# Kernel tuning notes

Measured on AMD Instinct MI355X. Metric: run time of the kernel, lower is better.

The kernel has to match this reference:

```python
import jax, jax.numpy as jnp
import numpy as np

N = 1_000_000   # samples
D_IN = 100      # covariate dim (cfg_density[0][0])
H = 64          # hidden dim
NUM_HEADS = 5   # t-bins [0,.2,.4,.6,.8,1.0]


def setup_inputs() -> dict:
    key = jax.random.key(0)
    ks = jax.random.split(key, 17)
    s = 0.05  # param scale for numerical stability (torch init is data-independent anyway)
    return {
        "t": jax.random.uniform(ks[0], (N,), dtype=jnp.float32),
        "x": jax.random.normal(ks[1], (N, D_IN), dtype=jnp.float32),
        # density feature MLP (two Linear+ReLU layers)
        "dW1": jax.random.normal(ks[2], (D_IN, H), dtype=jnp.float32) * s,
        "db1": jax.random.normal(ks[3], (H,), dtype=jnp.float32) * s,
        "dW2": jax.random.normal(ks[4], (H, H), dtype=jnp.float32) * s,
        "db2": jax.random.normal(ks[5], (H,), dtype=jnp.float32) * s,
        # 5 multi-head branches, each 3 Treat_Linear layers (istreat=1 since isenhance=1)
        "hw1": jax.random.normal(ks[6], (NUM_HEADS, H, H), dtype=jnp.float32) * s,
        "htw1": jax.random.normal(ks[7], (NUM_HEADS, H), dtype=jnp.float32) * s,
        "hb1": jax.random.normal(ks[8], (NUM_HEADS, H), dtype=jnp.float32) * s,
        "hw2": jax.random.normal(ks[9], (NUM_HEADS, H, H), dtype=jnp.float32) * s,
        "htw2": jax.random.normal(ks[10], (NUM_HEADS, H), dtype=jnp.float32) * s,
        "hb2": jax.random.normal(ks[11], (NUM_HEADS, H), dtype=jnp.float32) * s,
        "hw3": jax.random.normal(ks[12], (NUM_HEADS, H, 1), dtype=jnp.float32) * s,
        "htw3": jax.random.normal(ks[13], (NUM_HEADS, 1), dtype=jnp.float32) * s,
        "hb3": jax.random.normal(ks[14], (NUM_HEADS, 1), dtype=jnp.float32) * s,
    }


def reference(t, x, dW1, db1, dW2, db2,
              hw1, htw1, hb1, hw2, htw2, hb2, hw3, htw3, hb3):
    # hidden_features: Linear+ReLU, Linear+ReLU
    h = jax.nn.relu(x @ dW1 + db1)        # [N, H]
    h = jax.nn.relu(h @ dW2 + db2)        # [N, H]

    tt = t[:, None]                        # treatment column [N, 1]
    # bin index per row: t in [0.2*q, 0.2*(q+1)); last bin closed at 1.0
    bins = jnp.clip(jnp.floor(t * NUM_HEADS).astype(jnp.int32), 0, NUM_HEADS - 1)

    out = jnp.zeros((x.shape[0], 1), dtype=h.dtype)
    for q in range(NUM_HEADS):  # fixed small set of structurally-distinct heads
        # Treat_Linear layer 1: feat@W + t*tw + b, relu
        a = jax.nn.relu(h @ hw1[q] + tt * htw1[q] + hb1[q])
        # Treat_Linear layer 2
        a = jax.nn.relu(a @ hw2[q] + tt * htw2[q] + hb2[q])
        # last layer: no activation, islastlayer=1
        a = a @ hw3[q] + tt * htw3[q] + hb3[q]   # [N, 1]
        out = out + jnp.where((bins == q)[:, None], a, 0.0)
    return out  # Drnet returns (None, Q); g is None so we return Q
```

## Files before the change

kernel.cpp:

```cpp
#include <hip/hip_runtime.h>

typedef _Float16 f16;
typedef _Float16 f16x8 __attribute__((ext_vector_type(8)));
typedef float f32x4 __attribute__((ext_vector_type(4)));

#define NB 5
#define H 64
#define DIN 100
#define NT 256
#define MAIN_BLOCKS 512

#define FR_W1   0
#define FR_W2   1024
#define FR_HD   1536
#define FR_TOT  6656

__global__ __launch_bounds__(256)
void prepack_kernel(const float* __restrict__ dW1, const float* __restrict__ dW2,
                    const float* __restrict__ hw1, const float* __restrict__ hw2,
                    f16x8* __restrict__ pw)
{
    int F = blockIdx.x * 256 + threadIdx.x;
    if (F >= FR_TOT) return;
    int lane = F & 63, g = lane >> 4, c = lane & 15;
    const float* src;
    int s, mt, kmax;
    if (F < FR_W2) {
        int r = F; s = r >> 8; mt = (r >> 6) & 3; src = dW1; kmax = 100;
    } else if (F < FR_HD) {
        int r = F - FR_W2; s = r >> 8; mt = (r >> 6) & 3; src = dW2; kmax = 64;
    } else {
        int r = F - FR_HD; int ql = r >> 9; int q = ql >> 1; int l = ql & 1;
        int r2 = r & 511; s = r2 >> 8; mt = (r2 >> 6) & 3;
        src = (l ? hw2 : hw1) + q * 64 * 64; kmax = 64;
    }
    f16x8 v;
    #pragma unroll
    for (int e = 0; e < 8; ++e) {
        int k = 32 * s + 8 * g + e;
        int m = 16 * mt + c;
        float val = (k < kmax) ? src[k * 64 + m] : 0.0f;
        v[e] = (f16)val;
    }
    pw[F] = v;
}

__device__ __forceinline__ f32x4 mfma16(f16x8 a, f16x8 b, f32x4 c) {
    return __builtin_amdgcn_mfma_f32_16x16x32_f16(a, b, c, 0, 0, 0);
}

__global__ __launch_bounds__(NT, 2)
void drnet_main(const float* __restrict__ t, const float* __restrict__ x,
                const float* __restrict__ db1, const float* __restrict__ db2,
                const float* __restrict__ hb1, const float* __restrict__ htw1,
                const float* __restrict__ hb2, const float* __restrict__ htw2,
                const float* __restrict__ hw3, const float* __restrict__ htw3,
                const float* __restrict__ hb3,
                const f16x8* __restrict__ pw,
                float* __restrict__ out, int N, int nch)
{
    __shared__ float sb1f[H], sb2f[H];
    __shared__ float shb1[NB * H], shw1t[NB * H], shb2[NB * H], shw2t[NB * H], sw3f[NB * H];
    __shared__ float shtw3[NB], shb3[NB];
    __shared__ unsigned char sli[NT], sqv[NT];
    __shared__ float stv[NT];
    __shared__ int scnt[NB + 1], sbase[NB + 1];
    __shared__ __align__(16) unsigned char hbuf[4][2][2048];

    const int tid = threadIdx.x;
    const int lane = tid & 63;
    const int wv = tid >> 6;
    const int g = lane >> 4;
    const int row = lane & 15;

    for (int p = tid; p < H; p += NT) { sb1f[p] = db1[p]; sb2f[p] = db2[p]; }
    for (int p = tid; p < NB * H; p += NT) {
        shb1[p] = hb1[p];  shw1t[p] = htw1[p];
        shb2[p] = hb2[p];  shw2t[p] = htw2[p];
        sw3f[p] = hw3[p];
    }
    if (tid < NB) { shtw3[tid] = htw3[tid]; shb3[tid] = hb3[tid]; }

    f16x8 w1f[16], w2f[8];
    #pragma unroll
    for (int u = 0; u < 16; ++u) w1f[u] = pw[FR_W1 + u * 64 + lane];
    #pragma unroll
    for (int u = 0; u < 8; ++u)  w2f[u] = pw[FR_W2 + u * 64 + lane];

    for (int ch = blockIdx.x; ch < nch; ch += MAIN_BLOCKS) {
        __syncthreads();
        if (tid <= NB) scnt[tid] = 0;
        __syncthreads();
        const int i0 = ch * NT + tid;
        int q0 = NB; float tv0 = 0.f;
        if (i0 < N) {
            tv0 = t[i0];
            int b = (int)floorf(tv0 * 5.0f);
            q0 = min(max(b, 0), NB - 1);
        }
        int pos = atomicAdd(&scnt[q0], 1);
        __syncthreads();
        if (tid == 0) {
            int r = 0;
            #pragma unroll
            for (int b = 0; b <= NB; ++b) { sbase[b] = r; r += scnt[b]; }
        }
        __syncthreads();
        int sp = sbase[q0] + pos;
        sli[sp] = (unsigned char)tid; sqv[sp] = (unsigned char)q0; stv[sp] = tv0;
        __syncthreads();

        for (int j = 0; j < 4; ++j) {
            const int p0 = (wv * 4 + j) * 16;
            const int qlo = sqv[p0];
            if (qlo >= NB) continue;
            const int qhi = min((int)sqv[p0 + 15], NB - 1);
            const int li = sli[p0 + row];
            const int rq = sqv[p0 + row];
            const float rt = stv[p0 + row];
            const int iv = (rq < NB) ? (ch * NT + li) : (ch * NT);

            const float4* x4 = (const float4*)(x + (size_t)iv * DIN);
            f16x8 xf[4];
            #pragma unroll
            for (int s = 0; s < 3; ++s) {
                float4 a = x4[8 * s + 2 * g];
                float4 b = x4[8 * s + 2 * g + 1];
                xf[s][0] = (f16)a.x; xf[s][1] = (f16)a.y; xf[s][2] = (f16)a.z; xf[s][3] = (f16)a.w;
                xf[s][4] = (f16)b.x; xf[s][5] = (f16)b.y; xf[s][6] = (f16)b.z; xf[s][7] = (f16)b.w;
            }
            {
                float4 a = make_float4(0.f, 0.f, 0.f, 0.f);
                if (g == 0) a = x4[24];
                xf[3][0] = (f16)a.x; xf[3][1] = (f16)a.y; xf[3][2] = (f16)a.z; xf[3][3] = (f16)a.w;
                xf[3][4] = (f16)0.f; xf[3][5] = (f16)0.f; xf[3][6] = (f16)0.f; xf[3][7] = (f16)0.f;
            }
            const f32x4 zero = {0.f, 0.f, 0.f, 0.f};
            f32x4 acc[4] = {zero, zero, zero, zero};
            #pragma unroll
            for (int s = 0; s < 4; ++s)
                #pragma unroll
                for (int mt = 0; mt < 4; ++mt)
                    acc[mt] = mfma16(w1f[s * 4 + mt], xf[s], acc[mt]);

            unsigned char* hA = hbuf[wv][0];
            unsigned char* hB = hbuf[wv][1];
            #pragma unroll
            for (int mt = 0; mt < 4; ++mt) {
                const float* bb = &sb1f[16 * mt + 4 * g];
                union { f16 h[4]; unsigned long long u; } pk;
                #pragma unroll
                for (int r2 = 0; r2 < 4; ++r2) pk.h[r2] = (f16)fmaxf(acc[mt][r2] + bb[r2], 0.f);
                *(unsigned long long*)(hA + ((row * 128 + 32 * mt + 8 * g) ^ ((row & 7) << 4))) = pk.u;
            }

            f32x4 acc2[4] = {zero, zero, zero, zero};
            #pragma unroll
            for (int s = 0; s < 2; ++s) {
                f16x8 hf = *(const f16x8*)(hA + ((row * 128 + 64 * s + 16 * g) ^ ((row & 7) << 4)));
                #pragma unroll
                for (int mt = 0; mt < 4; ++mt)
                    acc2[mt] = mfma16(w2f[s * 4 + mt], hf, acc2[mt]);
            }
            #pragma unroll
            for (int mt = 0; mt < 4; ++mt) {
                const float* bb = &sb2f[16 * mt + 4 * g];
                union { f16 h[4]; unsigned long long u; } pk;
                #pragma unroll
                for (int r2 = 0; r2 < 4; ++r2) pk.h[r2] = (f16)fmaxf(acc2[mt][r2] + bb[r2], 0.f);
                *(unsigned long long*)(hB + ((row * 128 + 32 * mt + 8 * g) ^ ((row & 7) << 4))) = pk.u;
            }

            #pragma unroll 1
            for (int q = qlo; q <= qhi; ++q) {
                const f16x8* ph1 = pw + FR_HD + (q * 2 + 0) * 512;
                const f16x8* ph2 = pw + FR_HD + (q * 2 + 1) * 512;

                f32x4 a1[4] = {zero, zero, zero, zero};
                #pragma unroll
                for (int s = 0; s < 2; ++s) {
                    f16x8 hf = *(const f16x8*)(hB + ((row * 128 + 64 * s + 16 * g) ^ ((row & 7) << 4)));
                    #pragma unroll
                    for (int mt = 0; mt < 4; ++mt)
                        a1[mt] = mfma16(ph1[(s * 4 + mt) * 64 + lane], hf, a1[mt]);
                }
                #pragma unroll
                for (int mt = 0; mt < 4; ++mt) {
                    const float* bb = &shb1[q * 64 + 16 * mt + 4 * g];
                    const float* tw = &shw1t[q * 64 + 16 * mt + 4 * g];
                    union { f16 h[4]; unsigned long long u; } pk;
                    #pragma unroll
                    for (int r2 = 0; r2 < 4; ++r2)
                        pk.h[r2] = (f16)fmaxf(a1[mt][r2] + bb[r2] + rt * tw[r2], 0.f);
                    *(unsigned long long*)(hA + ((row * 128 + 32 * mt + 8 * g) ^ ((row & 7) << 4))) = pk.u;
                }

                f32x4 a2[4] = {zero, zero, zero, zero};
                #pragma unroll
                for (int s = 0; s < 2; ++s) {
                    f16x8 hf = *(const f16x8*)(hA + ((row * 128 + 64 * s + 16 * g) ^ ((row & 7) << 4)));
                    #pragma unroll
                    for (int mt = 0; mt < 4; ++mt)
                        a2[mt] = mfma16(ph2[(s * 4 + mt) * 64 + lane], hf, a2[mt]);
                }

                float partial = 0.f;
                #pragma unroll
                for (int mt = 0; mt < 4; ++mt) {
                    const float* bb = &shb2[q * 64 + 16 * mt + 4 * g];
                    const float* tw = &shw2t[q * 64 + 16 * mt + 4 * g];
                    const float* w3 = &sw3f[q * 64 + 16 * mt + 4 * g];
                    #pragma unroll
                    for (int r2 = 0; r2 < 4; ++r2) {
                        float v = fmaxf(a2[mt][r2] + bb[r2] + rt * tw[r2], 0.f);
                        partial += v * w3[r2];
                    }
                }
                partial += __shfl_xor(partial, 16, 64);
                partial += __shfl_xor(partial, 32, 64);
                if (lane < 16 && rq == q) {
                    out[ch * NT + li] = partial + rt * shtw3[q] + shb3[q];
                }
            }
        }
    }
}

extern "C" void kernel_launch(void* const* d_in, const int* in_sizes, int n_in,
                              void* d_out, int out_size, void* d_ws, size_t ws_size,
                              hipStream_t stream) {
    const float* t    = (const float*)d_in[0];
    const float* x    = (const float*)d_in[1];
    const float* dW1  = (const float*)d_in[2];
    const float* db1  = (const float*)d_in[3];
    const float* dW2  = (const float*)d_in[4];
    const float* db2  = (const float*)d_in[5];
    const float* hw1  = (const float*)d_in[6];
    const float* htw1 = (const float*)d_in[7];
    const float* hb1  = (const float*)d_in[8];
    const float* hw2  = (const float*)d_in[9];
    const float* htw2 = (const float*)d_in[10];
    const float* hb2  = (const float*)d_in[11];
    const float* hw3  = (const float*)d_in[12];
    const float* htw3 = (const float*)d_in[13];
    const float* hb3  = (const float*)d_in[14];
    float* out = (float*)d_out;

    const int N = in_sizes[0];
    const int nch = (N + NT - 1) / NT;
    f16x8* pw = (f16x8*)d_ws;

    prepack_kernel<<<(FR_TOT + 255) / 256, 256, 0, stream>>>(dW1, dW2, hw1, hw2, pw);
    drnet_main<<<MAIN_BLOCKS, NT, 0, stream>>>(t, x, db1, db2, hb1, htw1, hb2, htw2,
                                               hw3, htw3, hb3, pw, out, N, nch);
}
```

Before: 182.1 us.

## Prefetch next x tile into registers, stage outputs in LDS, raise occupancy

Each wave now loads the x rows for its next 16-row group into registers while it computes the current group, so global load latency is hidden behind the MFMA work. Outputs are gathered in a shared buffer and written back coalesced once per chunk, replacing scattered per-row stores. Occupancy is raised to 3 blocks per CU with a matching grid size. The leading barrier is dropped and the bin computation is simplified. These changes raise register pressure from the held prefetch buffers and could cause spills under the tighter launch bound. Removing the barrier at the top of the loop also adds a risk of races on the shared arrays between chunks.

```diff
diff --git a/kernel.cpp b/kernel.cpp
--- a/kernel.cpp
+++ b/kernel.cpp
@@ -8,7 +8,7 @@
 #define H 64
 #define DIN 100
 #define NT 256
-#define MAIN_BLOCKS 512
+#define MAIN_BLOCKS 768
 
 #define FR_W1   0
 #define FR_W2   1024
@@ -49,7 +49,7 @@
     return __builtin_amdgcn_mfma_f32_16x16x32_f16(a, b, c, 0, 0, 0);
 }
 
-__global__ __launch_bounds__(NT, 2)
+__global__ __launch_bounds__(NT, 3)
 void drnet_main(const float* __restrict__ t, const float* __restrict__ x,
                 const float* __restrict__ db1, const float* __restrict__ db2,
                 const float* __restrict__ hb1, const float* __restrict__ htw1,
@@ -64,6 +64,7 @@
     __shared__ float shtw3[NB], shb3[NB];
     __shared__ unsigned char sli[NT], sqv[NT];
     __shared__ float stv[NT];
+    __shared__ float sout[NT];
     __shared__ int scnt[NB + 1], sbase[NB + 1];
     __shared__ __align__(16) unsigned char hbuf[4][2][2048];
 
@@ -88,15 +89,13 @@
     for (int u = 0; u < 8; ++u)  w2f[u] = pw[FR_W2 + u * 64 + lane];
 
     for (int ch = blockIdx.x; ch < nch; ch += MAIN_BLOCKS) {
-        __syncthreads();
         if (tid <= NB) scnt[tid] = 0;
         __syncthreads();
         const int i0 = ch * NT + tid;
         int q0 = NB; float tv0 = 0.f;
         if (i0 < N) {
             tv0 = t[i0];
-            int b = (int)floorf(tv0 * 5.0f);
-            q0 = min(max(b, 0), NB - 1);
+            q0 = min((int)(tv0 * 5.0f), NB - 1);
         }
         int pos = atomicAdd(&scnt[q0], 1);
         __syncthreads();
@@ -109,33 +108,53 @@
         int sp = sbase[q0] + pos;
         sli[sp] = (unsigned char)tid; sqv[sp] = (unsigned char)q0; stv[sp] = tv0;
         __syncthreads();
+
+        float4 xr[7];
+        {
+            int pp = (wv * 4) * 16 + row;
+            int ivn = (sqv[pp] < NB) ? (ch * NT + sli[pp]) : (ch * NT);
+            const float4* x4 = (const float4*)(x + (size_t)ivn * DIN);
+            #pragma unroll
+            for (int s = 0; s < 3; ++s) { xr[2*s] = x4[8*s + 2*g]; xr[2*s+1] = x4[8*s + 2*g + 1]; }
+            xr[6] = x4[24];
+        }
 
         for (int j = 0; j < 4; ++j) {
             const int p0 = (wv * 4 + j) * 16;
             const int qlo = sqv[p0];
-            if (qlo >= NB) continue;
-            const int qhi = min((int)sqv[p0 + 15], NB - 1);
+            const int qhi = (qlo < NB) ? min((int)sqv[p0 + 15], NB - 1) : 0;
             const int li = sli[p0 + row];
             const int rq = sqv[p0 + row];
             const float rt = stv[p0 + row];
-            const int iv = (rq < NB) ? (ch * NT + li) : (ch * NT);
-
-            const float4* x4 = (const float4*)(x + (size_t)iv * DIN);
+
             f16x8 xf[4];
             #pragma unroll
             for (int s = 0; s < 3; ++s) {
-                float4 a = x4[8 * s + 2 * g];
-                float4 b = x4[8 * s + 2 * g + 1];
+                float4 a = xr[2*s], b = xr[2*s+1];
                 xf[s][0] = (f16)a.x; xf[s][1] = (f16)a.y; xf[s][2] = (f16)a.z; xf[s][3] = (f16)a.w;
                 xf[s][4] = (f16)b.x; xf[s][5] = (f16)b.y; xf[s][6] = (f16)b.z; xf[s][7] = (f16)b.w;
             }
             {
-                float4 a = make_float4(0.f, 0.f, 0.f, 0.f);
-                if (g == 0) a = x4[24];
-                xf[3][0] = (f16)a.x; xf[3][1] = (f16)a.y; xf[3][2] = (f16)a.z; xf[3][3] = (f16)a.w;
+                float4 a = xr[6];
+                const bool lo = (g == 0);
+                xf[3][0] = lo ? (f16)a.x : (f16)0.f; xf[3][1] = lo ? (f16)a.y : (f16)0.f;
+                xf[3][2] = lo ? (f16)a.z : (f16)0.f; xf[3][3] = lo ? (f16)a.w : (f16)0.f;
                 xf[3][4] = (f16)0.f; xf[3][5] = (f16)0.f; xf[3][6] = (f16)0.f; xf[3][7] = (f16)0.f;
             }
+
+            if (j < 3) {
+                int pp = (wv * 4 + j + 1) * 16 + row;
+                int ivn = (sqv[pp] < NB) ? (ch * NT + sli[pp]) : (ch * NT);
+                const float4* x4 = (const float4*)(x + (size_t)ivn * DIN);
+                #pragma unroll
+                for (int s = 0; s < 3; ++s) { xr[2*s] = x4[8*s + 2*g]; xr[2*s+1] = x4[8*s + 2*g + 1]; }
+                xr[6] = x4[24];
+            }
+
+            if (qlo >= NB) continue;
+
             const f32x4 zero = {0.f, 0.f, 0.f, 0.f};
+
             f32x4 acc[4] = {zero, zero, zero, zero};
             #pragma unroll
             for (int s = 0; s < 4; ++s)
@@ -219,9 +238,15 @@
                 partial += __shfl_xor(partial, 16, 64);
                 partial += __shfl_xor(partial, 32, 64);
                 if (lane < 16 && rq == q) {
-                    out[ch * NT + li] = partial + rt * shtw3[q] + shb3[q];
-                }
-            }
+                    sout[li] = partial + rt * shtw3[q] + shb3[q];
+                }
+            }
+        }
+
+        __syncthreads();
+        {
+            const int iw = ch * NT + tid;
+            if (iw < N) out[iw] = sout[tid];
         }
     }
 }
```

Result: slower. 215.4 us (+18.3%).

## Process two row tiles per wave, prefetch next t, and stage outputs in LDS

Applied to the files above, without the earlier changes.

Each wave now handles two 16-row tiles together. Their x loads are issued back to back and their MFMA chains are interleaved, which raises memory-level parallelism and gives the MFMA pipe independent work. The t value for the next chunk is prefetched during the current one, one block-level barrier is removed, and the bin index drops its floor and lower clamp. Outputs are gathered in shared memory and written out coalesced after a barrier rather than scattered to global memory. In exchange, register and LDS use rise, and a tile pair runs the union of both tiles' head range, so some head passes are redundant.

```diff
diff --git a/kernel.cpp b/kernel.cpp
--- a/kernel.cpp
+++ b/kernel.cpp
@@ -49,6 +49,36 @@
     return __builtin_amdgcn_mfma_f32_16x16x32_f16(a, b, c, 0, 0, 0);
 }
 
+__device__ __forceinline__ void epi_plain(unsigned char* buf, int row, int g,
+                                          const f32x4* acc, const float* bias) {
+    #pragma unroll
+    for (int mt = 0; mt < 4; ++mt) {
+        const float* bb = &bias[16 * mt + 4 * g];
+        union { f16 h[4]; unsigned long long u; } pk;
+        #pragma unroll
+        for (int r2 = 0; r2 < 4; ++r2) pk.h[r2] = (f16)fmaxf(acc[mt][r2] + bb[r2], 0.f);
+        *(unsigned long long*)(buf + ((row * 128 + 32 * mt + 8 * g) ^ ((row & 7) << 4))) = pk.u;
+    }
+}
+
+__device__ __forceinline__ void epi_t(unsigned char* buf, int row, int g, float rt,
+                                      const f32x4* acc, const float* bias, const float* tw) {
+    #pragma unroll
+    for (int mt = 0; mt < 4; ++mt) {
+        const float* bb = &bias[16 * mt + 4 * g];
+        const float* tt = &tw[16 * mt + 4 * g];
+        union { f16 h[4]; unsigned long long u; } pk;
+        #pragma unroll
+        for (int r2 = 0; r2 < 4; ++r2)
+            pk.h[r2] = (f16)fmaxf(acc[mt][r2] + bb[r2] + rt * tt[r2], 0.f);
+        *(unsigned long long*)(buf + ((row * 128 + 32 * mt + 8 * g) ^ ((row & 7) << 4))) = pk.u;
+    }
+}
+
+__device__ __forceinline__ f16x8 lds_read_h(const unsigned char* buf, int row, int g, int s) {
+    return *(const f16x8*)(buf + ((row * 128 + 64 * s + 16 * g) ^ ((row & 7) << 4)));
+}
+
 __global__ __launch_bounds__(NT, 2)
 void drnet_main(const float* __restrict__ t, const float* __restrict__ x,
                 const float* __restrict__ db1, const float* __restrict__ db2,
@@ -64,8 +94,9 @@
     __shared__ float shtw3[NB], shb3[NB];
     __shared__ unsigned char sli[NT], sqv[NT];
     __shared__ float stv[NT];
+    __shared__ float sout[NT];
     __shared__ int scnt[NB + 1], sbase[NB + 1];
-    __shared__ __align__(16) unsigned char hbuf[4][2][2048];
+    __shared__ __align__(16) unsigned char hbuf[4][2][2][2048];
 
     const int tid = threadIdx.x;
     const int lane = tid & 63;
@@ -87,17 +118,19 @@
     #pragma unroll
     for (int u = 0; u < 8; ++u)  w2f[u] = pw[FR_W2 + u * 64 + lane];
 
+    float tpre = 0.f;
+    {
+        int i0 = blockIdx.x * NT + tid;
+        if (blockIdx.x < nch && i0 < N) tpre = t[i0];
+    }
+
     for (int ch = blockIdx.x; ch < nch; ch += MAIN_BLOCKS) {
-        __syncthreads();
         if (tid <= NB) scnt[tid] = 0;
         __syncthreads();
         const int i0 = ch * NT + tid;
-        int q0 = NB; float tv0 = 0.f;
-        if (i0 < N) {
-            tv0 = t[i0];
-            int b = (int)floorf(tv0 * 5.0f);
-            q0 = min(max(b, 0), NB - 1);
-        }
+        const float tv0 = tpre;
+        int q0 = NB;
+        if (i0 < N) q0 = min((int)(tv0 * 5.0f), NB - 1);
         int pos = atomicAdd(&scnt[q0], 1);
         __syncthreads();
         if (tid == 0) {
@@ -110,101 +143,132 @@
         sli[sp] = (unsigned char)tid; sqv[sp] = (unsigned char)q0; stv[sp] = tv0;
         __syncthreads();
 
-        for (int j = 0; j < 4; ++j) {
-            const int p0 = (wv * 4 + j) * 16;
-            const int qlo = sqv[p0];
-            if (qlo >= NB) continue;
-            const int qhi = min((int)sqv[p0 + 15], NB - 1);
-            const int li = sli[p0 + row];
-            const int rq = sqv[p0 + row];
-            const float rt = stv[p0 + row];
-            const int iv = (rq < NB) ? (ch * NT + li) : (ch * NT);
-
-            const float4* x4 = (const float4*)(x + (size_t)iv * DIN);
-            f16x8 xf[4];
+        {
+            int inx = (ch + MAIN_BLOCKS) * NT + tid;
+            tpre = (ch + MAIN_BLOCKS < nch && inx < N) ? t[inx] : 0.f;
+        }
+
+        for (int j = 0; j < 2; ++j) {
+            const int pA = (wv * 4 + 2 * j) * 16;
+            const int pB = pA + 16;
+            const int qloA = sqv[pA];
+            const int qloB = sqv[pB];
+            const int liA = sli[pA + row], liB = sli[pB + row];
+            const int rqA = sqv[pA + row], rqB = sqv[pB + row];
+            const float rtA = stv[pA + row], rtB = stv[pB + row];
+            const int ivA = (rqA < NB) ? (ch * NT + liA) : (ch * NT);
+            const int ivB = (rqB < NB) ? (ch * NT + liB) : (ch * NT);
+
+            float4 xrA[7], xrB[7];
+            {
+                const float4* x4 = (const float4*)(x + (size_t)ivA * DIN);
+                #pragma unroll
+                for (int s = 0; s < 3; ++s) { xrA[2*s] = x4[8*s + 2*g]; xrA[2*s+1] = x4[8*s + 2*g + 1]; }
+                xrA[6] = x4[24];
+            }
+            {
+                const float4* x4 = (const float4*)(x + (size_t)ivB * DIN);
+                #pragma unroll
+                for (int s = 0; s < 3; ++s) { xrB[2*s] = x4[8*s + 2*g]; xrB[2*s+1] = x4[8*s + 2*g + 1]; }
+                xrB[6] = x4[24];
+            }
+
+            if (qloA >= NB) continue;
+
+            f16x8 xfA[4], xfB[4];
             #pragma unroll
             for (int s = 0; s < 3; ++s) {
-                float4 a = x4[8 * s + 2 * g];
-                float4 b = x4[8 * s + 2 * g + 1];
-                xf[s][0] = (f16)a.x; xf[s][1] = (f16)a.y; xf[s][2] = (f16)a.z; xf[s][3] = (f16)a.w;
-                xf[s][4] = (f16)b.x; xf[s][5] = (f16)b.y; xf[s][6] = (f16)b.z; xf[s][7] = (f16)b.w;
+                float4 a = xrA[2*s], b = xrA[2*s+1];
+                xfA[s][0]=(f16)a.x; xfA[s][1]=(f16)a.y; xfA[s][2]=(f16)a.z; xfA[s][3]=(f16)a.w;
+                xfA[s][4]=(f16)b.x; xfA[s][5]=(f16)b.y; xfA[s][6]=(f16)b.z; xfA[s][7]=(f16)b.w;
+                float4 c = xrB[2*s], d = xrB[2*s+1];
+                xfB[s][0]=(f16)c.x; xfB[s][1]=(f16)c.y; xfB[s][2]=(f16)c.z; xfB[s][3]=(f16)c.w;
+                xfB[s][4]=(f16)d.x; xfB[s][5]=(f16)d.y; xfB[s][6]=(f16)d.z; xfB[s][7]=(f16)d.w;
             }
             {
-                float4 a = make_float4(0.f, 0.f, 0.f, 0.f);
-                if (g == 0) a = x4[24];
-                xf[3][0] = (f16)a.x; xf[3][1] = (f16)a.y; xf[3][2] = (f16)a.z; xf[3][3] = (f16)a.w;
-                xf[3][4] = (f16)0.f; xf[3][5] = (f16)0.f; xf[3][6] = (f16)0.f; xf[3][7] = (f16)0.f;
-            }
+                const bool lo = (g == 0);
+                float4 a = xrA[6], b = xrB[6];
+                xfA[3][0]=lo?(f16)a.x:(f16)0.f; xfA[3][1]=lo?(f16)a.y:(f16)0.f;
+                xfA[3][2]=lo?(f16)a.z:(f16)0.f; xfA[3][3]=lo?(f16)a.w:(f16)0.f;
+                xfA[3][4]=(f16)0.f; xfA[3][5]=(f16)0.f; xfA[3][6]=(f16)0.f; xfA[3][7]=(f16)0.f;
+                xfB[3][0]=lo?(f16)b.x:(f16)0.f; xfB[3][1]=lo?(f16)b.y:(f16)0.f;
+                xfB[3][2]=lo?(f16)b.z:(f16)0.f; xfB[3][3]=lo?(f16)b.w:(f16)0.f;
+                xfB[3][4]=(f16)0.f; xfB[3][5]=(f16)0.f; xfB[3][6]=(f16)0.f; xfB[3][7]=(f16)0.f;
+            }
+
             const f32x4 zero = {0.f, 0.f, 0.f, 0.f};
-            f32x4 acc[4] = {zero, zero, zero, zero};
+            unsigned char* hA_A = hbuf[wv][0][0];
+            unsigned char* hB_A = hbuf[wv][0][1];
+            unsigned char* hA_B = hbuf[wv][1][0];
+            unsigned char* hB_B = hbuf[wv][1][1];
+
+            f32x4 accA[4] = {zero, zero, zero, zero};
+            f32x4 accB[4] = {zero, zero, zero, zero};
             #pragma unroll
             for (int s = 0; s < 4; ++s)
                 #pragma unroll
-                for (int mt = 0; mt < 4; ++mt)
-                    acc[mt] = mfma16(w1f[s * 4 + mt], xf[s], acc[mt]);
-
-            unsigned char* hA = hbuf[wv][0];
-            unsigned char* hB = hbuf[wv][1];
-            #pragma unroll
-            for (int mt = 0; mt < 4; ++mt) {
-                const float* bb = &sb1f[16 * mt + 4 * g];
-                union { f16 h[4]; unsigned long long u; } pk;
-                #pragma unroll
-                for (int r2 = 0; r2 < 4; ++r2) pk.h[r2] = (f16)fmaxf(acc[mt][r2] + bb[r2], 0.f);
-                *(unsigned long long*)(hA + ((row * 128 + 32 * mt + 8 * g) ^ ((row & 7) << 4))) = pk.u;
-            }
-
-            f32x4 acc2[4] = {zero, zero, zero, zero};
+                for (int mt = 0; mt < 4; ++mt) {
+                    accA[mt] = mfma16(w1f[s * 4 + mt], xfA[s], accA[mt]);
+                    accB[mt] = mfma16(w1f[s * 4 + mt], xfB[s], accB[mt]);
+                }
+            epi_plain(hA_A, row, g, accA, sb1f);
+            epi_plain(hA_B, row, g, accB, sb1f);
+
+            f32x4 acc2A[4] = {zero, zero, zero, zero};
+            f32x4 acc2B[4] = {zero, zero, zero, zero};
             #pragma unroll
             for (int s = 0; s < 2; ++s) {
-                f16x8 hf = *(const f16x8*)(hA + ((row * 128 + 64 * s + 16 * g) ^ ((row & 7) << 4)));
-                #pragma unroll
-                for (int mt = 0; mt < 4; ++mt)
-                    acc2[mt] = mfma16(w2f[s * 4 + mt], hf, acc2[mt]);
-            }
-            #pragma unroll
-            for (int mt = 0; mt < 4; ++mt) {
-                const float* bb = &sb2f[16 * mt + 4 * g];
-                union { f16 h[4]; unsigned long long u; } pk;
-                #pragma unroll
-                for (int r2 = 0; r2 < 4; ++r2) pk.h[r2] = (f16)fmaxf(acc2[mt][r2] + bb[r2], 0.f);
-                *(unsigned long long*)(hB + ((row * 128 + 32 * mt + 8 * g) ^ ((row & 7) << 4))) = pk.u;
-            }
+                f16x8 hfA = lds_read_h(hA_A, row, g, s);
+                f16x8 hfB = lds_read_h(hA_B, row, g, s);
+                #pragma unroll
+                for (int mt = 0; mt < 4; ++mt) {
+                    acc2A[mt] = mfma16(w2f[s * 4 + mt], hfA, acc2A[mt]);
+                    acc2B[mt] = mfma16(w2f[s * 4 + mt], hfB, acc2B[mt]);
+                }
+            }
+            epi_plain(hB_A, row, g, acc2A, sb2f);
+            epi_plain(hB_B, row, g, acc2B, sb2f);
+
+            const int qhiA = min((int)sqv[pA + 15], NB - 1);
+            int qhi = qhiA;
+            if (qloB < NB) qhi = max(qhi, min((int)sqv[pB + 15], NB - 1));
 
             #pragma unroll 1
-            for (int q = qlo; q <= qhi; ++q) {
+            for (int q = qloA; q <= qhi; ++q) {
                 const f16x8* ph1 = pw + FR_HD + (q * 2 + 0) * 512;
                 const f16x8* ph2 = pw + FR_HD + (q * 2 + 1) * 512;
 
-                f32x4 a1[4] = {zero, zero, zero, zero};
+                f32x4 a1A[4] = {zero, zero, zero, zero};
+                f32x4 a1B[4] = {zero, zero, zero, zero};
                 #pragma unroll
                 for (int s = 0; s < 2; ++s) {
-                    f16x8 hf = *(const f16x8*)(hB + ((row * 128 + 64 * s + 16 * g) ^ ((row & 7) << 4)));
+                    f16x8 hfA = lds_read_h(hB_A, row, g, s);
+                    f16x8 hfB = lds_read_h(hB_B, row, g, s);
                     #pragma unroll
-                    for (int mt = 0; mt < 4; ++mt)
-                        a1[mt] = mfma16(ph1[(s * 4 + mt) * 64 + lane], hf, a1[mt]);
-                }
-                #pragma unroll
-                for (int mt = 0; mt < 4; ++mt) {
-                    const float* bb = &shb1[q * 64 + 16 * mt + 4 * g];
-                    const float* tw = &shw1t[q * 64 + 16 * mt + 4 * g];
-                    union { f16 h[4]; unsigned long long u; } pk;
+                    for (int mt = 0; mt < 4; ++mt) {
+                        f16x8 wf = ph1[(s * 4 + mt) * 64 + lane];
+                        a1A[mt] = mfma16(wf, hfA, a1A[mt]);
+                        a1B[mt] = mfma16(wf, hfB, a1B[mt]);
+                    }
+                }
+                epi_t(hA_A, row, g, rtA, a1A, &shb1[q * 64], &shw1t[q * 64]);
+                epi_t(hA_B, row, g, rtB, a1B, &shb1[q * 64], &shw1t[q * 64]);
+
+                f32x4 a2A[4] = {zero, zero, zero, zero};
+                f32x4 a2B[4] = {zero, zero, zero, zero};
+                #pragma unroll
+                for (int s = 0; s < 2; ++s) {
+                    f16x8 hfA = lds_read_h(hA_A, row, g, s);
+                    f16x8 hfB = lds_read_h(hA_B, row, g, s);
                     #pragma unroll
-                    for (int r2 = 0; r2 < 4; ++r2)
-                        pk.h[r2] = (f16)fmaxf(a1[mt][r2] + bb[r2] + rt * tw[r2], 0.f);
-                    *(unsigned long long*)(hA + ((row * 128 + 32 * mt + 8 * g) ^ ((row & 7) << 4))) = pk.u;
-                }
-
-                f32x4 a2[4] = {zero, zero, zero, zero};
-                #pragma unroll
-                for (int s = 0; s < 2; ++s) {
-                    f16x8 hf = *(const f16x8*)(hA + ((row * 128 + 64 * s + 16 * g) ^ ((row & 7) << 4)));
-                    #pragma unroll
-                    for (int mt = 0; mt < 4; ++mt)
-                        a2[mt] = mfma16(ph2[(s * 4 + mt) * 64 + lane], hf, a2[mt]);
-                }
-
-                float partial = 0.f;
+                    for (int mt = 0; mt < 4; ++mt) {
+                        f16x8 wf = ph2[(s * 4 + mt) * 64 + lane];
+                        a2A[mt] = mfma16(wf, hfA, a2A[mt]);
+                        a2B[mt] = mfma16(wf, hfB, a2B[mt]);
+                    }
+                }
+
+                float pa = 0.f, pb = 0.f;
                 #pragma unroll
                 for (int mt = 0; mt < 4; ++mt) {
                     const float* bb = &shb2[q * 64 + 16 * mt + 4 * g];
@@ -212,16 +276,27 @@
                     const float* w3 = &sw3f[q * 64 + 16 * mt + 4 * g];
                     #pragma unroll
                     for (int r2 = 0; r2 < 4; ++r2) {
-                        float v = fmaxf(a2[mt][r2] + bb[r2] + rt * tw[r2], 0.f);
-                        partial += v * w3[r2];
+                        float vA = fmaxf(a2A[mt][r2] + bb[r2] + rtA * tw[r2], 0.f);
+                        float vB = fmaxf(a2B[mt][r2] + bb[r2] + rtB * tw[r2], 0.f);
+                        pa += vA * w3[r2];
+                        pb += vB * w3[r2];
                     }
                 }
-                partial += __shfl_xor(partial, 16, 64);
-                partial += __shfl_xor(partial, 32, 64);
-                if (lane < 16 && rq == q) {
-                    out[ch * NT + li] = partial + rt * shtw3[q] + shb3[q];
-                }
-            }
+                pa += __shfl_xor(pa, 16, 64);
+                pa += __shfl_xor(pa, 32, 64);
+                pb += __shfl_xor(pb, 16, 64);
+                pb += __shfl_xor(pb, 32, 64);
+                if (lane < 16) {
+                    if (rqA == q) sout[liA] = pa + rtA * shtw3[q] + shb3[q];
+                    if (rqB == q) sout[liB] = pb + rtB * shtw3[q] + shb3[q];
+                }
+            }
+        }
+
+        __syncthreads();
+        {
+            const int iw = ch * NT + tid;
+            if (iw < N) out[iw] = sout[tid];
         }
     }
 }
```

New measurement: 160.6 us. 11.8% less time.
